# Optimization experiments

Measured on AMD Instinct MI355X. Metric: run time of the kernel, lower is better.

Reference implementation:

```python
import jax, jax.numpy as jnp
import numpy as np

RESO = 32
PADDING = 0.02


def setup_inputs() -> dict:
    key = jax.random.key(0)
    ks = jax.random.split(key, 8)
    N, P, F, H, C = 8, 131072, 32, 128, 32
    return {
        "points": jax.random.uniform(ks[0], (N, P, 3), dtype=jnp.float32),
        "feature": jax.random.normal(ks[1], (N, P, F), dtype=jnp.float32),
        "fc0_w": jax.random.normal(ks[2], (F, F), dtype=jnp.float32) / np.sqrt(F),
        "fc0_b": jnp.zeros((F,), jnp.float32),
        "fc1_w": jax.random.normal(ks[3], (F, H), dtype=jnp.float32) / np.sqrt(F),
        "fc1_b": jnp.zeros((H,), jnp.float32),
        "sc_w": jax.random.normal(ks[4], (F, H), dtype=jnp.float32) / np.sqrt(F),
        "conv_w": jax.random.normal(ks[5], (C, H), dtype=jnp.float32) / np.sqrt(H),
        "conv_b": jnp.zeros((C,), jnp.float32),
    }


def _coord_to_index(points):
    # pad_and_crop_coordinate3d: shrink unit cube by padding, clip into [0,1)
    q = (points - 0.5) / (1.0 + PADDING + 1e-3) + 0.5
    q = jnp.clip(q, 0.0, 1.0 - 1e-6)
    xyz = (q * RESO).astype(jnp.int32)  # [N,P,3]
    idx = xyz[..., 0] + RESO * (xyz[..., 1] + RESO * xyz[..., 2])  # [N,P]
    return idx


def reference(points, feature, fc0_w, fc0_b, fc1_w, fc1_b, sc_w, conv_w, conv_b):
    N, P, _ = feature.shape
    H = fc1_w.shape[1]
    R3 = RESO ** 3

    idx = _coord_to_index(points)  # [N,P] int32

    # ResnetBlockFC: shortcut(x) + fc1(relu(fc0(relu(x))))
    a = jax.nn.relu(feature)
    net = jax.nn.relu(a @ fc0_w + fc0_b)
    h = feature @ sc_w + (net @ fc1_w + fc1_b)  # [N,P,H]

    # scatter_max into voxel bins (empty bins -> 0, torch_scatter convention)
    seg = (idx + jnp.arange(N, dtype=jnp.int32)[:, None] * R3).reshape(-1)
    pooled = jax.ops.segment_max(h.reshape(N * P, H), seg, num_segments=N * R3)
    pooled = jnp.where(jnp.isneginf(pooled), 0.0, pooled)
    grid = pooled.reshape(N, R3, H)  # [N,R3,H]

    # 1x1x1 Conv3d == per-voxel channel mix
    out = jnp.einsum('nvh,ch->nvc', grid, conv_w) + conv_b
    feature_grid = out.transpose(0, 2, 1).reshape(N, -1, RESO, RESO, RESO)
    index = idx[:, None, :]  # [N,1,P]
    return index, feature_grid
```

## Files before the change

### kernel.cpp

```cpp
#include <hip/hip_runtime.h>

#define RESO 32
#define R3   32768
#define NB   8
#define PP   131072
#define FF   32
#define HH   128
#define CC   32
#define CAP  64
#define NPTS (NB*PP)
#define NSEG (NB*R3)

typedef __attribute__((ext_vector_type(8))) __bf16 bf16x8;
typedef __attribute__((ext_vector_type(4))) float  f32x4;

__device__ __forceinline__ f32x4 MFMA(bf16x8 a, bf16x8 b, f32x4 c) {
    return __builtin_amdgcn_mfma_f32_16x16x32_bf16(a, b, c, 0, 0, 0);
}

__global__ __launch_bounds__(256) void lpbe_bin(
    const float* __restrict__ points,
    unsigned* __restrict__ count,
    unsigned* __restrict__ bucket,
    float* __restrict__ index_out)
{
    int gid = blockIdx.x * 256 + threadIdx.x;

    const float* pp = points + (size_t)gid * 3;
    float px = pp[0], py = pp[1], pz = pp[2];
    const float DIV = 1.021f;
    const float HIq = (float)(1.0 - 1e-6);
    float qx = (px - 0.5f)/DIV + 0.5f; qx = fminf(fmaxf(qx, 0.0f), HIq);
    float qy = (py - 0.5f)/DIV + 0.5f; qy = fminf(fmaxf(qy, 0.0f), HIq);
    float qz = (pz - 0.5f)/DIV + 0.5f; qz = fminf(fmaxf(qz, 0.0f), HIq);
    int xi = (int)(qx * 32.0f);
    int yi = (int)(qy * 32.0f);
    int zi = (int)(qz * 32.0f);
    int idx = xi + RESO*(yi + RESO*zi);

    index_out[gid] = (float)idx;

    int seg = (gid >> 17) * R3 + idx;
    unsigned slot = atomicAdd(&count[seg], 1u);
    if (slot < CAP) bucket[(size_t)seg * CAP + slot] = (unsigned)gid;
}

__global__ __launch_bounds__(256, 3) void lpbe_pool(
    const float* __restrict__ feature,
    const float* __restrict__ fc0_w, const float* __restrict__ fc0_b,
    const float* __restrict__ fc1_w, const float* __restrict__ fc1_b,
    const float* __restrict__ sc_w,
    const float* __restrict__ conv_w, const float* __restrict__ conv_b,
    const unsigned* __restrict__ count, const unsigned* __restrict__ bucket,
    float* __restrict__ out)
{
    __shared__ __bf16 s_bsc[8][64*8];
    __shared__ __bf16 s_bw1[8][64*8];
    __shared__ __bf16 s_w0f[2][64*8];
    __shared__ __bf16 s_pool[4][16*136];

    const int tid  = threadIdx.x;
    const int wv   = tid >> 6;
    const int lane = tid & 63;
    const int c16  = lane & 15;
    const int g    = lane >> 4;

    for (int nt = wv; nt < 8; nt += 4) {
        bf16x8 v, w;
        #pragma unroll
        for (int e = 0; e < 8; ++e) {
            int kn = 8*g + e;
            int ks = (e < 4) ? (4*g + e) : (16 + 4*g + e-4);
            v[e] = (__bf16)sc_w [kn*HH + 16*nt + c16];
            w[e] = (__bf16)fc1_w[ks*HH + 16*nt + c16];
        }
        *(bf16x8*)&s_bsc[nt][lane*8] = v;
        *(bf16x8*)&s_bw1[nt][lane*8] = w;
    }
    if (wv < 2) {
        bf16x8 v;
        #pragma unroll
        for (int e = 0; e < 8; ++e)
            v[e] = (__bf16)fc0_w[(8*g + e)*FF + 16*wv + c16];
        *(bf16x8*)&s_w0f[wv][lane*8] = v;
    }

    const f32x4 b0A = *(const f32x4*)&fc0_b[4*g];
    const f32x4 b0B = *(const f32x4*)&fc0_b[16 + 4*g];
    float b1v[8];
    #pragma unroll
    for (int nt = 0; nt < 8; ++nt) b1v[nt] = fc1_b[16*nt + c16];
    const float cb0 = conv_b[c16], cb1 = conv_b[16 + c16];
    __syncthreads();

    const int wgid = blockIdx.x * 4 + wv;
    const int tb16 = wgid * 16;
    __bf16* spool = s_pool[wv];

    int cntv = (int)count[tb16 + c16];
    if (cntv > CAP) cntv = CAP;

    unsigned pid0 = 0, pid1 = 0, pid2 = 0;
    int kA0 = 0, kB0 = 0, kA1 = 0, kB1 = 0, kA2 = 0, kB2 = 0;
    f32x4 fa0, fb0, fa1, fb1, fa2, fb2;

#define LOADP(PIDX, S) do {                                                  \
    int _Pv = (PIDX);                            \
    kA##S = __builtin_amdgcn_readlane(cntv, 2*_Pv);                          \
    kB##S = __builtin_amdgcn_readlane(cntv, 2*_Pv + 1);                      \
    unsigned _pid = bucket[(size_t)(tb16 + 2*_Pv + (c16 >> 3))*CAP           \
                           + (c16 & 7)];                                     \
    pid##S = _pid & (NPTS - 1);                       \
} while (0)

#define LOADF(S) do {                                                        \
    const float* _fp = feature + (size_t)pid##S * FF + 8*g;                  \
    fa##S = *(const f32x4*)_fp;                                              \
    fb##S = *(const f32x4*)(_fp + 4);                                        \
} while (0)

#define STEP(Q, S, SF) do {                                                  \
    const int _q = (Q);                                                      \
    const int _kA = kA##S, _kB = kB##S;                                      \
    if (_q < 5) LOADP(_q + 3, S);                                            \
    if (_q < 6) LOADF(SF);                                                   \
    float run[8];                                                            \
    _Pragma("unroll")                                                        \
    for (int nt = 0; nt < 8; ++nt) run[nt] = -3.0e38f;                       \
    int _km = _kA > _kB ? _kA : _kB;                                         \
    int _T  = (_km + 7) >> 3;                                                \
    for (int t = 0; t < _T; ++t) {                                           \
        f32x4 u0, u1;                                                        \
        if (t == 0) { u0 = fa##S; u1 = fb##S; }                              \
        else {                                                               \
            unsigned _pid = bucket[(size_t)(tb16 + 2*_q + (c16 >> 3))*CAP    \
                                   + 8*t + (c16 & 7)] & (NPTS - 1);          \
            const float* _fp = feature + (size_t)_pid * FF + 8*g;            \
            u0 = *(const f32x4*)_fp;                                         \
            u1 = *(const f32x4*)(_fp + 4);                                   \
        }                                                                    \
        bf16x8 ar, aw;                                                       \
        _Pragma("unroll")                                                    \
        for (int e = 0; e < 4; ++e) {                                        \
            ar[e]   = (__bf16)u0[e];            ar[4+e] = (__bf16)u1[e];     \
            aw[e]   = (__bf16)fmaxf(u0[e],0.f); aw[4+e] = (__bf16)fmaxf(u1[e],0.f); \
        }                                                                    \
        bf16x8 w00 = *(const bf16x8*)&s_w0f[0][lane*8];                      \
        bf16x8 w01 = *(const bf16x8*)&s_w0f[1][lane*8];                      \
        f32x4 zz = {0.f,0.f,0.f,0.f};                                        \
        f32x4 n0 = MFMA(w00, aw, zz);         \
        f32x4 n1 = MFMA(w01, aw, zz);         \
        bf16x8 an;                            \
        _Pragma("unroll")                                                    \
        for (int r = 0; r < 4; ++r) {                                        \
            an[r]   = (__bf16)fmaxf(n0[r] + b0A[r], 0.f);                    \
            an[4+r] = (__bf16)fmaxf(n1[r] + b0B[r], 0.f);                    \
        }                                                                    \
        f32x4 mv;                                                            \
        _Pragma("unroll")                                                    \
        for (int r = 0; r < 4; ++r) {                                        \
            int _sl = 8*t + 4*(g & 1) + r;                                   \
            mv[r] = (_sl < ((g < 2) ? _kA : _kB)) ? 0.f : -3.0e38f;          \
        }                                                                    \
        _Pragma("unroll")                                                    \
        for (int nt = 0; nt < 8; ++nt) {                                     \
            bf16x8 bs = *(const bf16x8*)&s_bsc[nt][lane*8];                  \
            bf16x8 bw = *(const bf16x8*)&s_bw1[nt][lane*8];                  \
            f32x4 acc = mv;                                                  \
            acc = MFMA(ar, bs, acc);                                         \
            acc = MFMA(an, bw, acc);                                         \
            run[nt] = fmaxf(run[nt],                                         \
                      fmaxf(fmaxf(acc[0],acc[1]), fmaxf(acc[2],acc[3])));    \
        }                                                                    \
    }                                                                        \
    _Pragma("unroll")                                                        \
    for (int nt = 0; nt < 8; ++nt) {                                         \
        float m = fmaxf(run[nt], __shfl_xor(run[nt], 16));                   \
        float sel = (((g < 2) ? _kA : _kB) == 0) ? 0.f : (m + b1v[nt]);      \
        if (g == 0)      spool[(2*_q  )*136 + 16*nt + c16] = (__bf16)sel;    \
        else if (g == 2) spool[(2*_q+1)*136 + 16*nt + c16] = (__bf16)sel;    \
    }                                                                        \
} while (0)

    LOADP(0, 0);
    LOADP(1, 1);
    LOADP(2, 2);
    LOADF(0);
    LOADF(1);

    STEP(0, 0, 2);
    STEP(1, 1, 0);
    STEP(2, 2, 1);
    STEP(3, 0, 2);
    STEP(4, 1, 0);
    STEP(5, 2, 1);
    STEP(6, 0, 2);
    STEP(7, 1, 0);

    bf16x8 cw0[4], cw1[4];
    #pragma unroll
    for (int kk = 0; kk < 4; ++kk) {
        f32x4 a0 = *(const f32x4*)&conv_w[(size_t)c16*HH      + 32*kk + 8*g];
        f32x4 a1 = *(const f32x4*)&conv_w[(size_t)c16*HH      + 32*kk + 8*g + 4];
        f32x4 c0 = *(const f32x4*)&conv_w[(size_t)(16+c16)*HH + 32*kk + 8*g];
        f32x4 c1 = *(const f32x4*)&conv_w[(size_t)(16+c16)*HH + 32*kk + 8*g + 4];
        #pragma unroll
        for (int e = 0; e < 4; ++e) {
            cw0[kk][e] = (__bf16)a0[e]; cw0[kk][4+e] = (__bf16)a1[e];
            cw1[kk][e] = (__bf16)c0[e]; cw1[kk][4+e] = (__bf16)c1[e];
        }
    }
    asm volatile("s_waitcnt lgkmcnt(0)" ::: "memory");
    f32x4 o0 = {cb0, cb0, cb0, cb0};
    f32x4 o1 = {cb1, cb1, cb1, cb1};
    #pragma unroll
    for (int kk = 0; kk < 4; ++kk) {
        bf16x8 ap = *(const bf16x8*)&spool[c16*136 + 32*kk + 8*g];
        o0 = MFMA(ap, cw0[kk], o0);
        o1 = MFMA(ap, cw1[kk], o1);
    }
    const int n  = tb16 >> 15;
    const int vb = tb16 & (R3 - 1);
    float* ob = out + (size_t)n*CC*R3 + (size_t)vb + 4*g;
    *(f32x4*)(ob + (size_t)c16*R3)        = o0;
    *(f32x4*)(ob + (size_t)(16 + c16)*R3) = o1;

#undef STEP
#undef LOADF
#undef LOADP
}

extern "C" void kernel_launch(void* const* d_in, const int* in_sizes, int n_in,
                              void* d_out, int out_size, void* d_ws, size_t ws_size,
                              hipStream_t stream)
{
    const float* points  = (const float*)d_in[0];
    const float* feature = (const float*)d_in[1];
    const float* fc0_w   = (const float*)d_in[2];
    const float* fc0_b   = (const float*)d_in[3];
    const float* fc1_w   = (const float*)d_in[4];
    const float* fc1_b   = (const float*)d_in[5];
    const float* sc_w    = (const float*)d_in[6];
    const float* conv_w  = (const float*)d_in[7];
    const float* conv_b  = (const float*)d_in[8];

    unsigned* count  = (unsigned*)d_ws;
    unsigned* bucket = count + NSEG;
    float* out0 = (float*)d_out;
    float* out1 = out0 + (size_t)NPTS;

    hipMemsetAsync(count, 0, (size_t)NSEG * sizeof(unsigned), stream);
    lpbe_bin <<<NPTS/256, 256, 0, stream>>>(points, count, bucket, out0);
    lpbe_pool<<<NSEG/64,  256, 0, stream>>>(feature, fc0_w, fc0_b, fc1_w, fc1_b,
                                            sc_w, conv_w, conv_b, count, bucket, out1);
}
```

Before: 184.3 us.

## Halve voxels per wave and share conv tiles across wave pairs

Each wave now pools 8 voxels instead of 16, so each block covers 32 voxels and the grid doubles in size. Pairs of waves write into a shared 16-voxel pooling tile, and after a block barrier only even waves run the final 1x1 conv MFMA and store. The aim is more parallelism and shorter per-wave serial chains, which should help latency hiding on the gather-heavy pooling. In exchange the weight staging into LDS is repeated across twice as many blocks, a __syncthreads is added, and half the waves sit idle during the conv step.

```diff
diff --git a/kernel.cpp b/kernel.cpp
--- a/kernel.cpp
+++ b/kernel.cpp
@@ -57,7 +57,7 @@
     __shared__ __bf16 s_bsc[8][64*8];
     __shared__ __bf16 s_bw1[8][64*8];
     __shared__ __bf16 s_w0f[2][64*8];
-    __shared__ __bf16 s_pool[4][16*136];
+    __shared__ __bf16 s_pool[2][16*136];
 
     const int tid  = threadIdx.x;
     const int wv   = tid >> 6;
@@ -93,22 +93,23 @@
     const float cb0 = conv_b[c16], cb1 = conv_b[16 + c16];
     __syncthreads();
 
-    const int wgid = blockIdx.x * 4 + wv;
-    const int tb16 = wgid * 16;
-    __bf16* spool = s_pool[wv];
-
-    int cntv = (int)count[tb16 + c16];
+    const int vb32 = blockIdx.x * 32;
+    const int tb8  = vb32 + wv * 8;
+    __bf16* spool  = s_pool[wv >> 1];
+    const int lrb  = (wv & 1) * 8;
+
+    int cntv = (int)count[tb8 + (c16 & 7)];
     if (cntv > CAP) cntv = CAP;
 
-    unsigned pid0 = 0, pid1 = 0, pid2 = 0;
-    int kA0 = 0, kB0 = 0, kA1 = 0, kB1 = 0, kA2 = 0, kB2 = 0;
-    f32x4 fa0, fb0, fa1, fb1, fa2, fb2;
+    unsigned pid0 = 0, pid1 = 0;
+    int kA0 = 0, kB0 = 0, kA1 = 0, kB1 = 0;
+    f32x4 fa0, fb0, fa1, fb1;
 
 #define LOADP(PIDX, S) do {                                                  \
-    int _Pv = (PIDX);                            \
+    int _Pv = (PIDX);                                   \
     kA##S = __builtin_amdgcn_readlane(cntv, 2*_Pv);                          \
     kB##S = __builtin_amdgcn_readlane(cntv, 2*_Pv + 1);                      \
-    unsigned _pid = bucket[(size_t)(tb16 + 2*_Pv + (c16 >> 3))*CAP           \
+    unsigned _pid = bucket[(size_t)(tb8 + 2*_Pv + (c16 >> 3))*CAP            \
                            + (c16 & 7)];                                     \
     pid##S = _pid & (NPTS - 1);                       \
 } while (0)
@@ -119,11 +120,11 @@
     fb##S = *(const f32x4*)(_fp + 4);                                        \
 } while (0)
 
-#define STEP(Q, S, SF) do {                                                  \
+#define STEP(Q, S, SN) do {                                                  \
     const int _q = (Q);                                                      \
     const int _kA = kA##S, _kB = kB##S;                                      \
-    if (_q < 5) LOADP(_q + 3, S);                                            \
-    if (_q < 6) LOADF(SF);                                                   \
+    if (_q < 2) LOADP(_q + 2, S);                     \
+    if (_q < 3) LOADF(SN);                        \
     float run[8];                                                            \
     _Pragma("unroll")                                                        \
     for (int nt = 0; nt < 8; ++nt) run[nt] = -3.0e38f;                       \
@@ -133,7 +134,7 @@
         f32x4 u0, u1;                                                        \
         if (t == 0) { u0 = fa##S; u1 = fb##S; }                              \
         else {                                                               \
-            unsigned _pid = bucket[(size_t)(tb16 + 2*_q + (c16 >> 3))*CAP    \
+            unsigned _pid = bucket[(size_t)(tb8 + 2*_q + (c16 >> 3))*CAP     \
                                    + 8*t + (c16 & 7)] & (NPTS - 1);          \
             const float* _fp = feature + (size_t)_pid * FF + 8*g;            \
             u0 = *(const f32x4*)_fp;                                         \
@@ -177,53 +178,53 @@
     for (int nt = 0; nt < 8; ++nt) {                                         \
         float m = fmaxf(run[nt], __shfl_xor(run[nt], 16));                   \
         float sel = (((g < 2) ? _kA : _kB) == 0) ? 0.f : (m + b1v[nt]);      \
-        if (g == 0)      spool[(2*_q  )*136 + 16*nt + c16] = (__bf16)sel;    \
-        else if (g == 2) spool[(2*_q+1)*136 + 16*nt + c16] = (__bf16)sel;    \
+        if (g == 0)      spool[(lrb + 2*_q    )*136 + 16*nt + c16] = (__bf16)sel; \
+        else if (g == 2) spool[(lrb + 2*_q + 1)*136 + 16*nt + c16] = (__bf16)sel; \
     }                                                                        \
 } while (0)
 
     LOADP(0, 0);
+    LOADF(0);
     LOADP(1, 1);
-    LOADP(2, 2);
-    LOADF(0);
-    LOADF(1);
-
-    STEP(0, 0, 2);
+
+    STEP(0, 0, 1);
     STEP(1, 1, 0);
-    STEP(2, 2, 1);
-    STEP(3, 0, 2);
-    STEP(4, 1, 0);
-    STEP(5, 2, 1);
-    STEP(6, 0, 2);
-    STEP(7, 1, 0);
-
-    bf16x8 cw0[4], cw1[4];
-    #pragma unroll
-    for (int kk = 0; kk < 4; ++kk) {
-        f32x4 a0 = *(const f32x4*)&conv_w[(size_t)c16*HH      + 32*kk + 8*g];
-        f32x4 a1 = *(const f32x4*)&conv_w[(size_t)c16*HH      + 32*kk + 8*g + 4];
-        f32x4 c0 = *(const f32x4*)&conv_w[(size_t)(16+c16)*HH + 32*kk + 8*g];
-        f32x4 c1 = *(const f32x4*)&conv_w[(size_t)(16+c16)*HH + 32*kk + 8*g + 4];
-        #pragma unroll
-        for (int e = 0; e < 4; ++e) {
-            cw0[kk][e] = (__bf16)a0[e]; cw0[kk][4+e] = (__bf16)a1[e];
-            cw1[kk][e] = (__bf16)c0[e]; cw1[kk][4+e] = (__bf16)c1[e];
+    STEP(2, 0, 1);
+    STEP(3, 1, 0);
+
+    __syncthreads();
+
+    if ((wv & 1) == 0) {
+        const int tile = wv >> 1;
+        const __bf16* tp = s_pool[tile];
+        bf16x8 cw0[4], cw1[4];
+        #pragma unroll
+        for (int kk = 0; kk < 4; ++kk) {
+            f32x4 a0 = *(const f32x4*)&conv_w[(size_t)c16*HH      + 32*kk + 8*g];
+            f32x4 a1 = *(const f32x4*)&conv_w[(size_t)c16*HH      + 32*kk + 8*g + 4];
+            f32x4 c0 = *(const f32x4*)&conv_w[(size_t)(16+c16)*HH + 32*kk + 8*g];
+            f32x4 c1 = *(const f32x4*)&conv_w[(size_t)(16+c16)*HH + 32*kk + 8*g + 4];
+            #pragma unroll
+            for (int e = 0; e < 4; ++e) {
+                cw0[kk][e] = (__bf16)a0[e]; cw0[kk][4+e] = (__bf16)a1[e];
+                cw1[kk][e] = (__bf16)c0[e]; cw1[kk][4+e] = (__bf16)c1[e];
+            }
         }
+        f32x4 o0 = {cb0, cb0, cb0, cb0};
+        f32x4 o1 = {cb1, cb1, cb1, cb1};
+        #pragma unroll
+        for (int kk = 0; kk < 4; ++kk) {
+            bf16x8 ap = *(const bf16x8*)&tp[c16*136 + 32*kk + 8*g];
+            o0 = MFMA(ap, cw0[kk], o0);
+            o1 = MFMA(ap, cw1[kk], o1);
+        }
+        const int tbase = vb32 + tile * 16;
+        const int n  = tbase >> 15;
+        const int vb = tbase & (R3 - 1);
+        float* ob = out + (size_t)n*CC*R3 + (size_t)vb + 4*g;
+        *(f32x4*)(ob + (size_t)c16*R3)        = o0;
+        *(f32x4*)(ob + (size_t)(16 + c16)*R3) = o1;
     }
-    asm volatile("s_waitcnt lgkmcnt(0)" ::: "memory");
-    f32x4 o0 = {cb0, cb0, cb0, cb0};
-    f32x4 o1 = {cb1, cb1, cb1, cb1};
-    #pragma unroll
-    for (int kk = 0; kk < 4; ++kk) {
-        bf16x8 ap = *(const bf16x8*)&spool[c16*136 + 32*kk + 8*g];
-        o0 = MFMA(ap, cw0[kk], o0);
-        o1 = MFMA(ap, cw1[kk], o1);
-    }
-    const int n  = tb16 >> 15;
-    const int vb = tb16 & (R3 - 1);
-    float* ob = out + (size_t)n*CC*R3 + (size_t)vb + 4*g;
-    *(f32x4*)(ob + (size_t)c16*R3)        = o0;
-    *(f32x4*)(ob + (size_t)(16 + c16)*R3) = o1;
 
 #undef STEP
 #undef LOADF
@@ -251,6 +252,6 @@
 
     hipMemsetAsync(count, 0, (size_t)NSEG * sizeof(unsigned), stream);
     lpbe_bin <<<NPTS/256, 256, 0, stream>>>(points, count, bucket, out0);
-    lpbe_pool<<<NSEG/64,  256, 0, stream>>>(feature, fc0_w, fc0_b, fc1_w, fc1_b,
+    lpbe_pool<<<NSEG/32,  256, 0, stream>>>(feature, fc0_w, fc0_b, fc1_w, fc1_b,
                                             sc_w, conv_w, conv_b, count, bucket, out1);
 }
```

Result: slower. 196.9 us (+6.8%).

## Reorder MFMA chain to overlap fc0 latency and shrink prefetch depth

Applied to the files above, without the earlier changes.

Issues the eight shortcut MFMAs right after the fc0 MFMAs so they hide fc0 latency before the relu/convert feeds the fc1 MFMAs, holding eight accumulators live. The software prefetch ring drops from three stages to two, with points and features loaded one pair ahead instead of two. This lowers register pressure from prefetch buffers but adds accumulator registers, and the shallower prefetch may expose more gather latency.

```diff
diff --git a/kernel.cpp b/kernel.cpp
--- a/kernel.cpp
+++ b/kernel.cpp
@@ -100,12 +100,12 @@
     int cntv = (int)count[tb16 + c16];
     if (cntv > CAP) cntv = CAP;
 
-    unsigned pid0 = 0, pid1 = 0, pid2 = 0;
-    int kA0 = 0, kB0 = 0, kA1 = 0, kB1 = 0, kA2 = 0, kB2 = 0;
-    f32x4 fa0, fb0, fa1, fb1, fa2, fb2;
+    unsigned pid0 = 0, pid1 = 0;
+    int kA0 = 0, kB0 = 0, kA1 = 0, kB1 = 0;
+    f32x4 fa0, fb0, fa1, fb1;
 
 #define LOADP(PIDX, S) do {                                                  \
-    int _Pv = (PIDX);                            \
+    int _Pv = (PIDX);                                   \
     kA##S = __builtin_amdgcn_readlane(cntv, 2*_Pv);                          \
     kB##S = __builtin_amdgcn_readlane(cntv, 2*_Pv + 1);                      \
     unsigned _pid = bucket[(size_t)(tb16 + 2*_Pv + (c16 >> 3))*CAP           \
@@ -119,11 +119,11 @@
     fb##S = *(const f32x4*)(_fp + 4);                                        \
 } while (0)
 
-#define STEP(Q, S, SF) do {                                                  \
+#define STEP(Q, S, SN) do {                                                  \
     const int _q = (Q);                                                      \
     const int _kA = kA##S, _kB = kB##S;                                      \
-    if (_q < 5) LOADP(_q + 3, S);                                            \
-    if (_q < 6) LOADF(SF);                                                   \
+    if (_q < 6) LOADP(_q + 2, S);                     \
+    if (_q < 7) LOADF(SN);                        \
     float run[8];                                                            \
     _Pragma("unroll")                                                        \
     for (int nt = 0; nt < 8; ++nt) run[nt] = -3.0e38f;                       \
@@ -150,27 +150,38 @@
         f32x4 zz = {0.f,0.f,0.f,0.f};                                        \
         f32x4 n0 = MFMA(w00, aw, zz);         \
         f32x4 n1 = MFMA(w01, aw, zz);         \
+        f32x4 mv;                                                            \
+        _Pragma("unroll")                                                    \
+        for (int r = 0; r < 4; ++r) {                                        \
+            int _sl = 8*t + 4*(g & 1) + r;                                   \
+            mv[r] = (_sl < ((g < 2) ? _kA : _kB)) ? 0.f : -3.0e38f;          \
+        }                                                                    \
+                          \
+        f32x4 acc[8];                                                        \
+        _Pragma("unroll")                                                    \
+        for (int nt = 0; nt < 8; ++nt) {                                     \
+            bf16x8 bs = *(const bf16x8*)&s_bsc[nt][lane*8];                  \
+            acc[nt] = MFMA(ar, bs, mv);                                      \
+        }                                                                    \
+                           \
         bf16x8 an;                            \
         _Pragma("unroll")                                                    \
         for (int r = 0; r < 4; ++r) {                                        \
             an[r]   = (__bf16)fmaxf(n0[r] + b0A[r], 0.f);                    \
             an[4+r] = (__bf16)fmaxf(n1[r] + b0B[r], 0.f);                    \
         }                                                                    \
-        f32x4 mv;                                                            \
-        _Pragma("unroll")                                                    \
-        for (int r = 0; r < 4; ++r) {                                        \
-            int _sl = 8*t + 4*(g & 1) + r;                                   \
-            mv[r] = (_sl < ((g < 2) ? _kA : _kB)) ? 0.f : -3.0e38f;          \
-        }                                                                    \
+           \
         _Pragma("unroll")                                                    \
         for (int nt = 0; nt < 8; ++nt) {                                     \
-            bf16x8 bs = *(const bf16x8*)&s_bsc[nt][lane*8];                  \
             bf16x8 bw = *(const bf16x8*)&s_bw1[nt][lane*8];                  \
-            f32x4 acc = mv;                                                  \
-            acc = MFMA(ar, bs, acc);                                         \
-            acc = MFMA(an, bw, acc);                                         \
+            acc[nt] = MFMA(an, bw, acc[nt]);                                 \
+        }                                                                    \
+                                                     \
+        _Pragma("unroll")                                                    \
+        for (int nt = 0; nt < 8; ++nt) {                                     \
             run[nt] = fmaxf(run[nt],                                         \
-                      fmaxf(fmaxf(acc[0],acc[1]), fmaxf(acc[2],acc[3])));    \
+                      fmaxf(fmaxf(acc[nt][0],acc[nt][1]),                    \
+                            fmaxf(acc[nt][2],acc[nt][3])));                  \
         }                                                                    \
     }                                                                        \
     _Pragma("unroll")                                                        \
@@ -183,18 +194,16 @@
 } while (0)
 
     LOADP(0, 0);
+    LOADF(0);
     LOADP(1, 1);
-    LOADP(2, 2);
-    LOADF(0);
-    LOADF(1);
-
-    STEP(0, 0, 2);
+
+    STEP(0, 0, 1);
     STEP(1, 1, 0);
-    STEP(2, 2, 1);
-    STEP(3, 0, 2);
-    STEP(4, 1, 0);
-    STEP(5, 2, 1);
-    STEP(6, 0, 2);
+    STEP(2, 0, 1);
+    STEP(3, 1, 0);
+    STEP(4, 0, 1);
+    STEP(5, 1, 0);
+    STEP(6, 0, 1);
     STEP(7, 1, 0);
 
     bf16x8 cw0[4], cw1[4];
```

Measured after the change: 203.2 us. 1.1x slower.
